# Kernel tuning notes

Measured on AMD Instinct MI355X. Metric: run time of the kernel, lower is better.

The kernel has to match this reference:

```python
import jax, jax.numpy as jnp
import numpy as np

TAU = 1.0
NUM_CLASSES = 14
LOSS_WEIGHT = 1.0


def setup_inputs() -> dict:
    key = jax.random.key(0)
    k1, k2, k3 = jax.random.split(key, 3)
    B, C, H, W = 8, NUM_CLASSES, 512, 512
    preds_S = jax.random.normal(k1, (B, C, H, W), dtype=jnp.float32)
    preds_T = jax.random.normal(k2, (B, C, H, W), dtype=jnp.float32)
    gt_labels = jax.random.randint(k3, (B, 1, H, W), 0, NUM_CLASSES, dtype=jnp.int32)
    return {"preds_S": preds_S, "preds_T": preds_T, "gt_labels": gt_labels}


def _boundaries(gt):
    # gt: [B, H, W] int. Per-class binary mask for classes 1..NUM_CLASSES-1,
    # boundary = mask XOR binary_erosion(mask) with cross (connectivity-1)
    # structuring element and zero border (scipy/cupy ndimage default).
    classes = jnp.arange(1, NUM_CLASSES, dtype=gt.dtype)  # [K]
    m = gt[:, None, :, :] == classes[None, :, None, None]  # [B, K, H, W] bool
    mp = jnp.pad(m, ((0, 0), (0, 0), (1, 1), (1, 1)))  # zero border
    eroded = (m
              & mp[:, :, :-2, 1:-1]   # up
              & mp[:, :, 2:, 1:-1]    # down
              & mp[:, :, 1:-1, :-2]   # left
              & mp[:, :, 1:-1, 2:])   # right
    return m ^ eroded  # [B, K, H, W] bool


def reference(preds_S, preds_T, gt_labels):
    B, C, H, W = preds_S.shape
    P = H * W
    dt = preds_S.dtype

    boundary = _boundaries(gt_labels[:, 0]).reshape(B, NUM_CLASSES - 1, P)
    bf = boundary.astype(dt)  # [B, K, P]

    # Channel-dim (dim=0 of the [C, HW] view) softmax is per-pixel, so
    # gathering boundary pixels then softmaxing == softmax everywhere + mask.
    log_pS = jax.nn.log_softmax(preds_S / TAU, axis=1).reshape(B, C, P)
    log_pT = jax.nn.log_softmax(preds_T / TAU, axis=1).reshape(B, C, P)
    pT = jnp.exp(log_pT)
    # pointwise KL summed over channels, per pixel: [B, P]
    kl_pix = jnp.sum(pT * (log_pT - log_pS), axis=1)

    n = jnp.sum(bf, axis=-1)                              # [B, K] boundary sizes
    kl_sum = jnp.einsum('bkp,bp->bk', bf, kl_pix)         # [B, K]
    # Original skips when idxs.sum() == 0, i.e. sum of flat boundary indices
    # is zero (no boundary pixels, or sole boundary pixel at index 0).
    idx = jnp.arange(P, dtype=dt)
    idx_sum = jnp.einsum('bkp,p->bk', bf, idx)            # [B, K]
    valid = idx_sum > 0
    # F.kl_div reduction='mean' divides by total elements = C * n
    terms = jnp.where(valid, kl_sum / (C * jnp.maximum(n, 1.0)), 0.0)
    loss = LOSS_WEIGHT * (TAU ** 2) * jnp.sum(terms)
    return loss
```

## Files before the change

### kernel.cpp

```cpp
#include <hip/hip_runtime.h>


#define CC 14
#define KB 13
#define BB 8
#define HH 512
#define WW 512
#define PP (HH * WW)
#define PIX_PER_BLOCK 1024
#define BLOCKS_PER_IMG (PP / PIX_PER_BLOCK)

#define NBINS (BB * KB)

__global__ void zero_ws_kernel(float* __restrict__ ws) {
    int i = threadIdx.x;
    if (i < 2 * NBINS) ws[i] = 0.0f;
}

__global__ __launch_bounds__(256) void boundary_kl_kernel(
        const float* __restrict__ S, const float* __restrict__ T,
        const int* __restrict__ gt, float* __restrict__ ws) {
    const int tid = threadIdx.x;
    const int b   = blockIdx.x / BLOCKS_PER_IMG;
    const int p0  = (blockIdx.x % BLOCKS_PER_IMG) * PIX_PER_BLOCK + tid * 4;

    __shared__ float s_kl[KB + 1];
    __shared__ float s_n[KB + 1];
    if (tid <= KB) { s_kl[tid] = 0.0f; s_n[tid] = 0.0f; }
    __syncthreads();

    const float* Sb = S + (size_t)b * CC * PP + p0;
    const float* Tb = T + (size_t)b * CC * PP + p0;
    const int*  gtb = gt + (size_t)b * PP;

    float4 zS = make_float4(0.f, 0.f, 0.f, 0.f);
    float4 zT = make_float4(0.f, 0.f, 0.f, 0.f);
    float4 A  = make_float4(0.f, 0.f, 0.f, 0.f);
#pragma unroll 4
    for (int c = 0; c < CC; ++c) {
        const float4 xs = *(const float4*)(Sb + (size_t)c * PP);
        const float4 xt = *(const float4*)(Tb + (size_t)c * PP);
        const float4 eS = make_float4(__expf(xs.x), __expf(xs.y), __expf(xs.z), __expf(xs.w));
        const float4 eT = make_float4(__expf(xt.x), __expf(xt.y), __expf(xt.z), __expf(xt.w));
        zS.x += eS.x; zS.y += eS.y; zS.z += eS.z; zS.w += eS.w;
        zT.x += eT.x; zT.y += eT.y; zT.z += eT.z; zT.w += eT.w;
        A.x = fmaf(eT.x, xt.x - xs.x, A.x);
        A.y = fmaf(eT.y, xt.y - xs.y, A.y);
        A.z = fmaf(eT.z, xt.z - xs.z, A.z);
        A.w = fmaf(eT.w, xt.w - xs.w, A.w);
    }

    float kl[4];
    kl[0] = __fdividef(A.x, zT.x) + __logf(zS.x) - __logf(zT.x);
    kl[1] = __fdividef(A.y, zT.y) + __logf(zS.y) - __logf(zT.y);
    kl[2] = __fdividef(A.z, zT.z) + __logf(zS.z) - __logf(zT.z);
    kl[3] = __fdividef(A.w, zT.w) + __logf(zS.w) - __logf(zT.w);

    const int h = p0 >> 9;
    const int w = p0 & (WW - 1);
    int4 g = *(const int4*)(gtb + p0);
    int4 gu = make_int4(-1, -1, -1, -1);
    int4 gd = make_int4(-1, -1, -1, -1);
    if (h > 0)      gu = *(const int4*)(gtb + p0 - WW);
    if (h < HH - 1) gd = *(const int4*)(gtb + p0 + WW);
    const int gl = (w > 0)       ? gtb[p0 - 1] : -1;
    const int gr = (w + 4 < WW)  ? gtb[p0 + 4] : -1;

    const int gc[4]  = {g.x, g.y, g.z, g.w};
    const int gup[4] = {gu.x, gu.y, gu.z, gu.w};
    const int gdn[4] = {gd.x, gd.y, gd.z, gd.w};
    const int glf[4] = {gl, g.x, g.y, g.z};
    const int grt[4] = {g.y, g.z, g.w, gr};

#pragma unroll
    for (int j = 0; j < 4; ++j) {
        const int k = gc[j];
        const bool eroded = (glf[j] == k) & (grt[j] == k) & (gup[j] == k) & (gdn[j] == k);
        if (k >= 1 && !eroded) {
            atomicAdd(&s_kl[k], kl[j]);
            atomicAdd(&s_n[k], 1.0f);
        }
    }
    __syncthreads();

    if (tid >= 1 && tid <= KB) {
        atomicAdd(&ws[b * KB + (tid - 1)], s_kl[tid]);
        atomicAdd(&ws[NBINS + b * KB + (tid - 1)], s_n[tid]);
    }
}

__global__ void finalize_kernel(const float* __restrict__ ws,
                                const int* __restrict__ gt,
                                float* __restrict__ out) {
    __shared__ float partial[128];
    const int tid = threadIdx.x;
    float t = 0.0f;
    if (tid < NBINS) {
        const int b = tid / KB;
        const int k = (tid % KB) + 1;
        const float kl = ws[tid];
        const float n  = ws[NBINS + tid];
        const int k0 = gt[(size_t)b * PP];
        const float sub = (k0 == k) ? 1.0f : 0.0f;
        const float npos = n - sub;
        t = (npos > 0.0f) ? (kl / ((float)CC * fmaxf(n, 1.0f))) : 0.0f;
    }
    partial[tid] = t;
    __syncthreads();
    for (int s = 64; s > 0; s >>= 1) {
        if (tid < s) partial[tid] += partial[tid + s];
        __syncthreads();
    }
    if (tid == 0) out[0] = partial[0];
}

extern "C" void kernel_launch(void* const* d_in, const int* in_sizes, int n_in,
                              void* d_out, int out_size, void* d_ws, size_t ws_size,
                              hipStream_t stream) {
    const float* S  = (const float*)d_in[0];
    const float* T  = (const float*)d_in[1];
    const int*   gt = (const int*)d_in[2];
    float* out = (float*)d_out;
    float* ws  = (float*)d_ws;

    hipLaunchKernelGGL(zero_ws_kernel, dim3(1), dim3(256), 0, stream, ws);
    hipLaunchKernelGGL(boundary_kl_kernel, dim3(BB * BLOCKS_PER_IMG), dim3(256), 0, stream,
                       S, T, gt, ws);
    hipLaunchKernelGGL(finalize_kernel, dim3(1), dim3(128), 0, stream, ws, gt, out);
}
```

Baseline: 258.4 us.

## Stage channel loads through LDS with async global_load_lds pipeline

Replaces the direct float4 global loads of the 14 channels with asynchronous global-to-LDS copies into a four-slot ring buffer per wavefront. Manual s_waitcnt vmcnt fences keep three channels in flight while the current one is consumed from LDS. The aim is to hide memory latency in this bandwidth-bound KL reduction. The cost is 32 KB of LDS per block, which may lower occupancy, plus extra LDS reads and reliance on exact vmcnt accounting, which is fragile if the compiler inserts other vector memory ops.

Measured after the change: 257.9 us. About the same (-0.2%).

```diff
diff --git a/kernel.cpp b/kernel.cpp
--- a/kernel.cpp
+++ b/kernel.cpp
@@ -17,12 +17,21 @@
     if (i < 2 * NBINS) ws[i] = 0.0f;
 }
 
+__device__ __forceinline__ void stage16(const float* g, const float* l) {
+    __builtin_amdgcn_global_load_lds(
+        (const __attribute__((address_space(1))) void*)g,
+        (__attribute__((address_space(3))) void*)l,
+        16, 0, 0);
+}
+
 __global__ __launch_bounds__(256) void boundary_kl_kernel(
         const float* __restrict__ S, const float* __restrict__ T,
         const int* __restrict__ gt, float* __restrict__ ws) {
     const int tid = threadIdx.x;
     const int b   = blockIdx.x / BLOCKS_PER_IMG;
     const int p0  = (blockIdx.x % BLOCKS_PER_IMG) * PIX_PER_BLOCK + tid * 4;
+
+    __shared__ float lds[4 * 4 * 512];
 
     __shared__ float s_kl[KB + 1];
     __shared__ float s_n[KB + 1];
@@ -33,22 +42,52 @@
     const float* Tb = T + (size_t)b * CC * PP + p0;
     const int*  gtb = gt + (size_t)b * PP;
 
+    const int wslot = (tid >> 6) * 2048;
+    const int lofs  = (tid & 63) * 4;
+
     float4 zS = make_float4(0.f, 0.f, 0.f, 0.f);
     float4 zT = make_float4(0.f, 0.f, 0.f, 0.f);
     float4 A  = make_float4(0.f, 0.f, 0.f, 0.f);
-#pragma unroll 4
-    for (int c = 0; c < CC; ++c) {
-        const float4 xs = *(const float4*)(Sb + (size_t)c * PP);
-        const float4 xt = *(const float4*)(Tb + (size_t)c * PP);
-        const float4 eS = make_float4(__expf(xs.x), __expf(xs.y), __expf(xs.z), __expf(xs.w));
-        const float4 eT = make_float4(__expf(xt.x), __expf(xt.y), __expf(xt.z), __expf(xt.w));
-        zS.x += eS.x; zS.y += eS.y; zS.z += eS.z; zS.w += eS.w;
-        zT.x += eT.x; zT.y += eT.y; zT.z += eT.z; zT.w += eT.w;
-        A.x = fmaf(eT.x, xt.x - xs.x, A.x);
-        A.y = fmaf(eT.y, xt.y - xs.y, A.y);
-        A.z = fmaf(eT.z, xt.z - xs.z, A.z);
-        A.w = fmaf(eT.w, xt.w - xs.w, A.w);
-    }
+
+#define STAGE(c) do {                                                        \
+        stage16(Sb + (size_t)(c) * PP, &lds[wslot + ((c) & 3) * 512]);       \
+        stage16(Tb + (size_t)(c) * PP, &lds[wslot + ((c) & 3) * 512 + 256]); \
+    } while (0)
+
+#define CONSUME(c) do {                                                       \
+        const float4 xs = *(const float4*)&lds[wslot + ((c) & 3) * 512 + lofs];       \
+        const float4 xt = *(const float4*)&lds[wslot + ((c) & 3) * 512 + 256 + lofs]; \
+        const float4 eS = make_float4(__expf(xs.x), __expf(xs.y), __expf(xs.z), __expf(xs.w)); \
+        const float4 eT = make_float4(__expf(xt.x), __expf(xt.y), __expf(xt.z), __expf(xt.w)); \
+        zS.x += eS.x; zS.y += eS.y; zS.z += eS.z; zS.w += eS.w;               \
+        zT.x += eT.x; zT.y += eT.y; zT.z += eT.z; zT.w += eT.w;               \
+        A.x = fmaf(eT.x, xt.x - xs.x, A.x);                                   \
+        A.y = fmaf(eT.y, xt.y - xs.y, A.y);                                   \
+        A.z = fmaf(eT.z, xt.z - xs.z, A.z);                                   \
+        A.w = fmaf(eT.w, xt.w - xs.w, A.w);                                   \
+    } while (0)
+
+#define WAITVM(n) asm volatile("s_waitcnt vmcnt(" #n ")" ::: "memory")
+
+    STAGE(0); STAGE(1); STAGE(2);
+    STAGE(3);  WAITVM(6); CONSUME(0);
+    STAGE(4);  WAITVM(6); CONSUME(1);
+    STAGE(5);  WAITVM(6); CONSUME(2);
+    STAGE(6);  WAITVM(6); CONSUME(3);
+    STAGE(7);  WAITVM(6); CONSUME(4);
+    STAGE(8);  WAITVM(6); CONSUME(5);
+    STAGE(9);  WAITVM(6); CONSUME(6);
+    STAGE(10); WAITVM(6); CONSUME(7);
+    STAGE(11); WAITVM(6); CONSUME(8);
+    STAGE(12); WAITVM(6); CONSUME(9);
+    STAGE(13); WAITVM(6); CONSUME(10);
+    WAITVM(4); CONSUME(11);
+    WAITVM(2); CONSUME(12);
+    WAITVM(0); CONSUME(13);
+
+#undef STAGE
+#undef CONSUME
+#undef WAITVM
 
     float kl[4];
     kl[0] = __fdividef(A.x, zT.x) + __logf(zS.x) - __logf(zT.x);
```

## Process two pixel groups per thread and fuse finalize via last-block reduction

Applied to the files above, without the earlier changes.

Each thread now handles two float4 pixel groups (2048 pixels per block), which halves the block count and raises memory-level parallelism per thread, with the channel loop no longer unrolled. The separate finalize kernel is removed: a global atomic counter picks the last block to finish, and that block performs the final per-class reduction after thread fences. This drops one kernel launch and adds a counter atomic plus fences to every block.

Result: slower. 327.8 us (+26.9%).

```diff
diff --git a/kernel.cpp b/kernel.cpp
--- a/kernel.cpp
+++ b/kernel.cpp
@@ -7,111 +7,142 @@
 #define HH 512
 #define WW 512
 #define PP (HH * WW)
-#define PIX_PER_BLOCK 1024
+#define PIX_PER_BLOCK 2048
 #define BLOCKS_PER_IMG (PP / PIX_PER_BLOCK)
+#define NBLOCKS (BB * BLOCKS_PER_IMG)
 
 #define NBINS (BB * KB)
 
 __global__ void zero_ws_kernel(float* __restrict__ ws) {
     int i = threadIdx.x;
-    if (i < 2 * NBINS) ws[i] = 0.0f;
+    if (i < 2 * NBINS + 1) ws[i] = 0.0f;
 }
 
 __global__ __launch_bounds__(256) void boundary_kl_kernel(
         const float* __restrict__ S, const float* __restrict__ T,
-        const int* __restrict__ gt, float* __restrict__ ws) {
+        const int* __restrict__ gt, float* __restrict__ ws,
+        float* __restrict__ out) {
     const int tid = threadIdx.x;
     const int b   = blockIdx.x / BLOCKS_PER_IMG;
-    const int p0  = (blockIdx.x % BLOCKS_PER_IMG) * PIX_PER_BLOCK + tid * 4;
+    const int base = (blockIdx.x % BLOCKS_PER_IMG) * PIX_PER_BLOCK;
+    const int p0  = base + tid * 4;
+    const int p1  = p0 + 1024;
 
     __shared__ float s_kl[KB + 1];
     __shared__ float s_n[KB + 1];
     if (tid <= KB) { s_kl[tid] = 0.0f; s_n[tid] = 0.0f; }
     __syncthreads();
 
-    const float* Sb = S + (size_t)b * CC * PP + p0;
-    const float* Tb = T + (size_t)b * CC * PP + p0;
+    const float* Sb = S + (size_t)b * CC * PP;
+    const float* Tb = T + (size_t)b * CC * PP;
     const int*  gtb = gt + (size_t)b * PP;
 
-    float4 zS = make_float4(0.f, 0.f, 0.f, 0.f);
-    float4 zT = make_float4(0.f, 0.f, 0.f, 0.f);
-    float4 A  = make_float4(0.f, 0.f, 0.f, 0.f);
-#pragma unroll 4
+    float4 zS0 = make_float4(0.f,0.f,0.f,0.f), zT0 = zS0, A0 = zS0;
+    float4 zS1 = zS0, zT1 = zS0, A1 = zS0;
+#pragma unroll 1
     for (int c = 0; c < CC; ++c) {
-        const float4 xs = *(const float4*)(Sb + (size_t)c * PP);
-        const float4 xt = *(const float4*)(Tb + (size_t)c * PP);
-        const float4 eS = make_float4(__expf(xs.x), __expf(xs.y), __expf(xs.z), __expf(xs.w));
-        const float4 eT = make_float4(__expf(xt.x), __expf(xt.y), __expf(xt.z), __expf(xt.w));
-        zS.x += eS.x; zS.y += eS.y; zS.z += eS.z; zS.w += eS.w;
-        zT.x += eT.x; zT.y += eT.y; zT.z += eT.z; zT.w += eT.w;
-        A.x = fmaf(eT.x, xt.x - xs.x, A.x);
-        A.y = fmaf(eT.y, xt.y - xs.y, A.y);
-        A.z = fmaf(eT.z, xt.z - xs.z, A.z);
-        A.w = fmaf(eT.w, xt.w - xs.w, A.w);
+        const size_t co = (size_t)c * PP;
+        const float4 xs0 = *(const float4*)(Sb + co + p0);
+        const float4 xt0 = *(const float4*)(Tb + co + p0);
+        const float4 xs1 = *(const float4*)(Sb + co + p1);
+        const float4 xt1 = *(const float4*)(Tb + co + p1);
+
+        float4 e;
+        e = make_float4(__expf(xs0.x), __expf(xs0.y), __expf(xs0.z), __expf(xs0.w));
+        zS0.x += e.x; zS0.y += e.y; zS0.z += e.z; zS0.w += e.w;
+        e = make_float4(__expf(xt0.x), __expf(xt0.y), __expf(xt0.z), __expf(xt0.w));
+        zT0.x += e.x; zT0.y += e.y; zT0.z += e.z; zT0.w += e.w;
+        A0.x = fmaf(e.x, xt0.x - xs0.x, A0.x);
+        A0.y = fmaf(e.y, xt0.y - xs0.y, A0.y);
+        A0.z = fmaf(e.z, xt0.z - xs0.z, A0.z);
+        A0.w = fmaf(e.w, xt0.w - xs0.w, A0.w);
+
+        e = make_float4(__expf(xs1.x), __expf(xs1.y), __expf(xs1.z), __expf(xs1.w));
+        zS1.x += e.x; zS1.y += e.y; zS1.z += e.z; zS1.w += e.w;
+        e = make_float4(__expf(xt1.x), __expf(xt1.y), __expf(xt1.z), __expf(xt1.w));
+        zT1.x += e.x; zT1.y += e.y; zT1.z += e.z; zT1.w += e.w;
+        A1.x = fmaf(e.x, xt1.x - xs1.x, A1.x);
+        A1.y = fmaf(e.y, xt1.y - xs1.y, A1.y);
+        A1.z = fmaf(e.z, xt1.z - xs1.z, A1.z);
+        A1.w = fmaf(e.w, xt1.w - xs1.w, A1.w);
     }
 
-    float kl[4];
-    kl[0] = __fdividef(A.x, zT.x) + __logf(zS.x) - __logf(zT.x);
-    kl[1] = __fdividef(A.y, zT.y) + __logf(zS.y) - __logf(zT.y);
-    kl[2] = __fdividef(A.z, zT.z) + __logf(zS.z) - __logf(zT.z);
-    kl[3] = __fdividef(A.w, zT.w) + __logf(zS.w) - __logf(zT.w);
+    float kl0[4], kl1[4];
+    kl0[0] = __fdividef(A0.x, zT0.x) + __logf(zS0.x) - __logf(zT0.x);
+    kl0[1] = __fdividef(A0.y, zT0.y) + __logf(zS0.y) - __logf(zT0.y);
+    kl0[2] = __fdividef(A0.z, zT0.z) + __logf(zS0.z) - __logf(zT0.z);
+    kl0[3] = __fdividef(A0.w, zT0.w) + __logf(zS0.w) - __logf(zT0.w);
+    kl1[0] = __fdividef(A1.x, zT1.x) + __logf(zS1.x) - __logf(zT1.x);
+    kl1[1] = __fdividef(A1.y, zT1.y) + __logf(zS1.y) - __logf(zT1.y);
+    kl1[2] = __fdividef(A1.z, zT1.z) + __logf(zS1.z) - __logf(zT1.z);
+    kl1[3] = __fdividef(A1.w, zT1.w) + __logf(zS1.w) - __logf(zT1.w);
 
-    const int h = p0 >> 9;
-    const int w = p0 & (WW - 1);
-    int4 g = *(const int4*)(gtb + p0);
-    int4 gu = make_int4(-1, -1, -1, -1);
-    int4 gd = make_int4(-1, -1, -1, -1);
-    if (h > 0)      gu = *(const int4*)(gtb + p0 - WW);
-    if (h < HH - 1) gd = *(const int4*)(gtb + p0 + WW);
-    const int gl = (w > 0)       ? gtb[p0 - 1] : -1;
-    const int gr = (w + 4 < WW)  ? gtb[p0 + 4] : -1;
+#define BOUNDARY_BIN(q, kl) do {                                              \
+        const int h = (q) >> 9;                                               \
+        const int w = (q) & (WW - 1);                                         \
+        int4 g = *(const int4*)(gtb + (q));                                   \
+        int4 gu = make_int4(-1, -1, -1, -1);                                  \
+        int4 gd = make_int4(-1, -1, -1, -1);                                  \
+        if (h > 0)      gu = *(const int4*)(gtb + (q) - WW);                  \
+        if (h < HH - 1) gd = *(const int4*)(gtb + (q) + WW);                  \
+        const int gl = (w > 0)      ? gtb[(q) - 1] : -1;                      \
+        const int gr = (w + 4 < WW) ? gtb[(q) + 4] : -1;                      \
+        const int gc[4]  = {g.x, g.y, g.z, g.w};                              \
+        const int gup[4] = {gu.x, gu.y, gu.z, gu.w};                          \
+        const int gdn[4] = {gd.x, gd.y, gd.z, gd.w};                          \
+        const int glf[4] = {gl, g.x, g.y, g.z};                               \
+        const int grt[4] = {g.y, g.z, g.w, gr};                               \
+        _Pragma("unroll")                                                     \
+        for (int j = 0; j < 4; ++j) {                                         \
+            const int k = gc[j];                                              \
+            const bool er = (glf[j] == k) & (grt[j] == k) &                   \
+                            (gup[j] == k) & (gdn[j] == k);                    \
+            if (k >= 1 && !er) {                                              \
+                atomicAdd(&s_kl[k], (kl)[j]);                                 \
+                atomicAdd(&s_n[k], 1.0f);                                     \
+            }                                                                 \
+        }                                                                     \
+    } while (0)
 
-    const int gc[4]  = {g.x, g.y, g.z, g.w};
-    const int gup[4] = {gu.x, gu.y, gu.z, gu.w};
-    const int gdn[4] = {gd.x, gd.y, gd.z, gd.w};
-    const int glf[4] = {gl, g.x, g.y, g.z};
-    const int grt[4] = {g.y, g.z, g.w, gr};
-
-#pragma unroll
-    for (int j = 0; j < 4; ++j) {
-        const int k = gc[j];
-        const bool eroded = (glf[j] == k) & (grt[j] == k) & (gup[j] == k) & (gdn[j] == k);
-        if (k >= 1 && !eroded) {
-            atomicAdd(&s_kl[k], kl[j]);
-            atomicAdd(&s_n[k], 1.0f);
-        }
-    }
+    BOUNDARY_BIN(p0, kl0);
+    BOUNDARY_BIN(p1, kl1);
+#undef BOUNDARY_BIN
     __syncthreads();
 
     if (tid >= 1 && tid <= KB) {
         atomicAdd(&ws[b * KB + (tid - 1)], s_kl[tid]);
         atomicAdd(&ws[NBINS + b * KB + (tid - 1)], s_n[tid]);
     }
-}
 
-__global__ void finalize_kernel(const float* __restrict__ ws,
-                                const int* __restrict__ gt,
-                                float* __restrict__ out) {
-    __shared__ float partial[128];
-    const int tid = threadIdx.x;
-    float t = 0.0f;
-    if (tid < NBINS) {
-        const int b = tid / KB;
-        const int k = (tid % KB) + 1;
-        const float kl = ws[tid];
-        const float n  = ws[NBINS + tid];
-        const int k0 = gt[(size_t)b * PP];
-        const float sub = (k0 == k) ? 1.0f : 0.0f;
-        const float npos = n - sub;
-        t = (npos > 0.0f) ? (kl / ((float)CC * fmaxf(n, 1.0f))) : 0.0f;
+    __threadfence();
+    __shared__ bool is_last;
+    if (tid == 0) {
+        unsigned prev = atomicAdd((unsigned*)(ws + 2 * NBINS), 1u);
+        is_last = (prev == (unsigned)(NBLOCKS - 1));
     }
-    partial[tid] = t;
     __syncthreads();
-    for (int s = 64; s > 0; s >>= 1) {
-        if (tid < s) partial[tid] += partial[tid + s];
+    if (is_last) {
+        __threadfence();
+        __shared__ float partial[128];
+        float t = 0.0f;
+        if (tid < NBINS) {
+            const int b2 = tid / KB;
+            const int k  = (tid % KB) + 1;
+            const float kl = ws[tid];
+            const float n  = ws[NBINS + tid];
+            const int k0 = gt[(size_t)b2 * PP];
+            const float sub = (k0 == k) ? 1.0f : 0.0f;
+            const float npos = n - sub;
+            t = (npos > 0.0f) ? (kl / ((float)CC * fmaxf(n, 1.0f))) : 0.0f;
+        }
+        if (tid < 128) partial[tid] = t;
         __syncthreads();
+        for (int s = 64; s > 0; s >>= 1) {
+            if (tid < s) partial[tid] += partial[tid + s];
+            __syncthreads();
+        }
+        if (tid == 0) out[0] = partial[0];
     }
-    if (tid == 0) out[0] = partial[0];
 }
 
 extern "C" void kernel_launch(void* const* d_in, const int* in_sizes, int n_in,
@@ -124,7 +155,6 @@
     float* ws  = (float*)d_ws;
 
     hipLaunchKernelGGL(zero_ws_kernel, dim3(1), dim3(256), 0, stream, ws);
-    hipLaunchKernelGGL(boundary_kl_kernel, dim3(BB * BLOCKS_PER_IMG), dim3(256), 0, stream,
-                       S, T, gt, ws);
-    hipLaunchKernelGGL(finalize_kernel, dim3(1), dim3(128), 0, stream, ws, gt, out);
+    hipLaunchKernelGGL(boundary_kl_kernel, dim3(NBLOCKS), dim3(256), 0, stream,
+                       S, T, gt, ws, out);
 }
```
